# Kernel optimization log

Measured on AMD Instinct MI355X. Metric: run time of the kernel, lower is better.

## Reference

```python
import jax, jax.numpy as jnp
import numpy as np

B, E, DIN, H, D, T = 16, 512, 1024, 8, 128, 3
NEG = -1e30
LRELU_SLOPE = 0.2


def setup_inputs() -> dict:
    key = jax.random.key(0)
    ks = jax.random.split(key, 6)
    x = jax.random.normal(ks[0], (B, E, DIN), dtype=jnp.float32)
    adj = jax.random.randint(ks[1], (B, E, E), 0, 4, dtype=jnp.int32)  # 0=no edge, 1..3 edge types
    node_mask = jnp.ones((B, E, 1), dtype=jnp.float32)
    W = jax.random.normal(ks[2], (H, T, DIN, D), dtype=jnp.float32) * 0.02
    a1 = jax.random.normal(ks[3], (H, T, D), dtype=jnp.float32) * 0.02  # a[:d]
    a2 = jax.random.normal(ks[4], (H, T, D), dtype=jnp.float32) * 0.02  # a[d:]
    return {"x": x, "adj": adj, "node_mask": node_mask, "W": W, "a1": a1, "a2": a2}


def reference(x, adj, node_mask, W, a1, a2):
    # h per head/type: [H, T, B, E, D]
    h = jnp.einsum('bei,htid->htbed', x, W)
    # a(cat(h_i, h_j)) = h_i . a1 + h_j . a2 (linear, no bias)
    left = jnp.einsum('htbed,htd->htbe', h, a1)   # [H,T,B,E]
    right = jnp.einsum('htbed,htd->htbe', h, a2)  # [H,T,B,E]
    score = left[..., :, None] + right[..., None, :]             # [H,T,B,E,E]
    score = jnp.where(score > 0, score, LRELU_SLOPE * score)      # LeakyReLU(0.2)
    type_ids = (jnp.arange(T, dtype=adj.dtype) + 1).reshape(1, T, 1, 1, 1)
    # sum over types: only positions where adj == type contribute
    scores = jnp.sum(jnp.where(adj[None, None] == type_ids, score, 0.0), axis=1)  # [H,B,E,E]
    scores = jnp.where(adj[None] > 0, scores, NEG)
    coefs = jax.nn.softmax(scores, axis=-1)                       # [H,B,E,E]
    # original bug (faithful): h used in aggregation is from the LAST edge type
    h_last = h[:, -1] * node_mask[None]                           # [H,B,E,D]
    out = jnp.einsum('hbef,hbfd->hbed', coefs, h_last)            # [H,B,E,D]
    out = jnp.transpose(out, (1, 2, 0, 3)).reshape(B, E, H * D)   # concat heads
    return jax.nn.relu(out)
```

## Files before the change

### kernel.cpp

```cpp
#include <hip/hip_runtime.h>

typedef __attribute__((ext_vector_type(8))) _Float16 half8;
typedef __attribute__((ext_vector_type(8))) unsigned short u16x8;
typedef __attribute__((ext_vector_type(4))) unsigned short u16x4;
typedef __attribute__((ext_vector_type(4))) float f32x4;

#define NEGV (-1e30f)


__device__ __forceinline__ unsigned short f2h(float f) {
    union { _Float16 h; unsigned short u; } c;
    c.h = (_Float16)f;
    return c.u;
}
__device__ __forceinline__ float h2f(unsigned short u) {
    union { _Float16 h; unsigned short u; } c;
    c.u = u;
    return (float)c.h;
}

__global__ __launch_bounds__(256) void pack_all(const float* __restrict__ W,
                                                const float* __restrict__ a1,
                                                const float* __restrict__ a2,
                                                unsigned short* __restrict__ Bf) {
    __shared__ float tile[64 * 133];
    const int bid = blockIdx.x;
    const int tid = threadIdx.x;

    if (bid < 128) {
        const int kt = bid & 15, h = bid >> 4;
        const int k0 = kt * 64;
        const float* wsrc = W + ((size_t)((h * 3 + 2) * 1024) + k0) * 128;

        #pragma unroll
        for (int rep = 0; rep < 8; ++rep) {
            int idx = rep * 256 + tid;
            int k = idx >> 5, dc = (idx & 31) * 4;
            float4 v = *(const float4*)(wsrc + (size_t)k * 128 + dc);
            tile[k * 133 + dc + 0] = v.x;
            tile[k * 133 + dc + 1] = v.y;
            tile[k * 133 + dc + 2] = v.z;
            tile[k * 133 + dc + 3] = v.w;
        }
        __syncthreads();
        #pragma unroll
        for (int rep = 0; rep < 4; ++rep) {
            int idx = rep * 256 + tid;
            int d = idx >> 3, kc = (idx & 7) * 8;
            u16x8 vh;
            #pragma unroll
            for (int q = 0; q < 8; ++q) vh[q] = f2h(tile[(kc + q) * 133 + d]);
            *(u16x8*)(Bf + (size_t)(h * 128 + d) * 1024 + k0 + kc) = vh;
        }
    } else if (bid < 512) {
        const int b2 = bid - 128;
        const int kt = b2 & 15, ht = b2 >> 4;
        const int h = ht & 7, t = ht >> 3;
        const int k0 = kt * 64;
        const float* wsrc = W + ((size_t)((h * 3 + t) * 1024) + k0) * 128;

        #pragma unroll
        for (int rep = 0; rep < 8; ++rep) {
            int idx = rep * 256 + tid;
            int k = idx >> 5, dc = (idx & 31) * 4;
            float4 v = *(const float4*)(wsrc + (size_t)k * 128 + dc);
            tile[k * 133 + dc + 0] = v.x;
            tile[k * 133 + dc + 1] = v.y;
            tile[k * 133 + dc + 2] = v.z;
            tile[k * 133 + dc + 3] = v.w;
        }
        __syncthreads();
        if (tid < 128) {
            const int k = tid & 63, s = tid >> 6;
            const float* ar = (s ? a2 : a1) + (h * 3 + t) * 128;
            float acc = 0.f;
            #pragma unroll 4
            for (int d = 0; d < 128; ++d) acc += tile[k * 133 + d] * ar[d];
            Bf[(size_t)(1024 + s * 24 + t * 8 + h) * 1024 + k0 + k] = f2h(acc);
        }
    } else {
        const int n = 1072 + (bid - 512);
        *(unsigned long long*)(Bf + (size_t)n * 1024 + tid * 4) = 0ull;
    }
}

__global__ __launch_bounds__(256, 3) void mgemm(const float* __restrict__ X,
                                                const unsigned short* __restrict__ Bf,
                                                const float* __restrict__ nm,
                                                unsigned short* __restrict__ Vt,
                                                float* __restrict__ LR) {
    __shared__ unsigned short Ah[128 * 32];
    __shared__ unsigned short Al[128 * 32];
    __shared__ unsigned short Bfs[128 * 32];

    const int bid = blockIdx.x;
    const int swz = (bid & 7) * 72 + (bid >> 3);
    const int nt = swz % 9, mt = swz / 9;
    const int n0 = nt * 128, m0 = mt * 128;

    const int tid = threadIdx.x;
    const int lane = tid & 63, w = tid >> 6;
    const int wr = w >> 1, wc = w & 1;
    const int fr = lane & 15, fq = lane >> 4;

    f32x4 acc[4][4];
    #pragma unroll
    for (int m = 0; m < 4; ++m)
        #pragma unroll
        for (int n = 0; n < 4; ++n) acc[m][n] = (f32x4){0.f, 0.f, 0.f, 0.f};

    const int arow = tid >> 1, ahalf = tid & 1;
    const float* xs = X + (size_t)(m0 + arow) * 1024 + ahalf * 16;
    unsigned short* adh = Ah + arow * 32 + ahalf * 16;
    unsigned short* adl = Al + arow * 32 + ahalf * 16;

    for (int k0 = 0; k0 < 1024; k0 += 32) {
        __syncthreads();

        #pragma unroll
        for (int q = 0; q < 2; ++q) {
            const int s = q * 256 + tid;
            const int brow = s >> 2, bkb = s & 3;
            const unsigned short* g = Bf + (size_t)(n0 + brow) * 1024 + k0 + bkb * 8;
            unsigned short* d = Bfs + (q * 256 + w * 64) * 8;
            __builtin_amdgcn_global_load_lds(
                (const __attribute__((address_space(1))) void*)g,
                (__attribute__((address_space(3))) void*)d, 16, 0, 0);
        }

        float xf[16];
        #pragma unroll
        for (int i = 0; i < 4; ++i) {
            float4 v = *(const float4*)(xs + k0 + i * 4);
            xf[i * 4 + 0] = v.x; xf[i * 4 + 1] = v.y;
            xf[i * 4 + 2] = v.z; xf[i * 4 + 3] = v.w;
        }
        u16x8 vh0, vh1, vl0, vl1;
        #pragma unroll
        for (int i = 0; i < 8; ++i) {
            unsigned short hi = f2h(xf[i]);
            vh0[i] = hi;
            vl0[i] = f2h(xf[i] - h2f(hi));
        }
        #pragma unroll
        for (int i = 0; i < 8; ++i) {
            unsigned short hi = f2h(xf[8 + i]);
            vh1[i] = hi;
            vl1[i] = f2h(xf[8 + i] - h2f(hi));
        }
        *(u16x8*)(adh) = vh0;
        *(u16x8*)(adh + 8) = vh1;
        *(u16x8*)(adl) = vl0;
        *(u16x8*)(adl + 8) = vl1;

        __syncthreads();

        half8 amh[4], bn[4];
        #pragma unroll
        for (int m = 0; m < 4; ++m)
            amh[m] = *(half8*)(Ah + (wr * 64 + m * 16 + fr) * 32 + fq * 8);
        #pragma unroll
        for (int n = 0; n < 4; ++n)
            bn[n] = *(half8*)(Bfs + (wc * 64 + n * 16 + fr) * 32 + fq * 8);
        #pragma unroll
        for (int m = 0; m < 4; ++m)
            #pragma unroll
            for (int n = 0; n < 4; ++n)
                acc[m][n] = __builtin_amdgcn_mfma_f32_16x16x32_f16(amh[m], bn[n], acc[m][n], 0, 0, 0);

        half8 aml[4];
        #pragma unroll
        for (int m = 0; m < 4; ++m)
            aml[m] = *(half8*)(Al + (wr * 64 + m * 16 + fr) * 32 + fq * 8);
        #pragma unroll
        for (int m = 0; m < 4; ++m)
            #pragma unroll
            for (int n = 0; n < 4; ++n)
                acc[m][n] = __builtin_amdgcn_mfma_f32_16x16x32_f16(aml[m], bn[n], acc[m][n], 0, 0, 0);
    }

    if (nt < 8) {
        const int b_ = (mt * 128) >> 9;
        const int jb0 = (mt & 3) * 128;
        unsigned short* vtw = Vt + (size_t)(nt * 16 + b_) * 128 * 512;
        #pragma unroll
        for (int m = 0; m < 4; ++m) {
            const int jb = jb0 + wr * 64 + m * 16 + fq * 4;
            float mk[4];
            #pragma unroll
            for (int r = 0; r < 4; ++r)
                mk[r] = nm[m0 + wr * 64 + m * 16 + fq * 4 + r];
            #pragma unroll
            for (int n = 0; n < 4; ++n) {
                const int d = wc * 64 + n * 16 + fr;
                u16x4 pk;
                #pragma unroll
                for (int r = 0; r < 4; ++r) pk[r] = f2h(acc[m][n][r] * mk[r]);
                *(u16x4*)(vtw + (size_t)d * 512 + jb) = pk;
            }
        }
    } else {
        #pragma unroll
        for (int m = 0; m < 4; ++m) {
            #pragma unroll
            for (int r = 0; r < 4; ++r) {
                const int R = m0 + wr * 64 + m * 16 + fq * 4 + r;
                #pragma unroll
                for (int n = 0; n < 4; ++n) {
                    const int c = wc * 64 + n * 16 + fr;
                    if (c < 48) LR[(size_t)c * 8192 + R] = acc[m][n][r];
                }
            }
        }
    }
}

__global__ __launch_bounds__(256) void adjb_kernel(const int* __restrict__ adj,
                                                   unsigned char* __restrict__ adjB) {
    const int idx = blockIdx.x * 256 + threadIdx.x;
    const int4* s = (const int4*)(adj + (size_t)idx * 16);
    int4 v0 = s[0], v1 = s[1], v2 = s[2], v3 = s[3];
    union { unsigned char c[16]; int4 v; } o;
    o.c[0] = (unsigned char)v0.x; o.c[1] = (unsigned char)v0.y;
    o.c[2] = (unsigned char)v0.z; o.c[3] = (unsigned char)v0.w;
    o.c[4] = (unsigned char)v1.x; o.c[5] = (unsigned char)v1.y;
    o.c[6] = (unsigned char)v1.z; o.c[7] = (unsigned char)v1.w;
    o.c[8] = (unsigned char)v2.x; o.c[9] = (unsigned char)v2.y;
    o.c[10] = (unsigned char)v2.z; o.c[11] = (unsigned char)v2.w;
    o.c[12] = (unsigned char)v3.x; o.c[13] = (unsigned char)v3.y;
    o.c[14] = (unsigned char)v3.z; o.c[15] = (unsigned char)v3.w;
    *(int4*)(adjB + (size_t)idx * 16) = o.v;
}

__global__ __launch_bounds__(256, 4) void attn_kernel(const unsigned short* __restrict__ Vt,
                                                      const float* __restrict__ LR,
                                                      const unsigned char* __restrict__ adjB,
                                                      float* __restrict__ out) {
    __shared__ __align__(16) unsigned short Vb[2][16 * 512];
    __shared__ __align__(16) float rt[3 * 512];

    const int bid = blockIdx.x;
    const int itg = bid >> 7, hb = bid & 127, h = hb >> 4, b = hb & 15;
    const int tid = threadIdx.x, w = tid >> 6, lane = tid & 63;
    const int fr = lane & 15, fq = lane >> 4;
    const int i0 = (itg * 4 + w) * 16;
    const int fq8 = fq * 8;

    for (int idx = tid; idx < 1536; idx += 256) {
        int t = idx >> 9, j = idx & 511;
        rt[idx] = LR[(size_t)(24 + t * 8 + h) * 8192 + b * 512 + j];
    }
    const float lf0 = LR[(size_t)(h) * 8192 + b * 512 + i0 + fr];
    const float lf1 = LR[(size_t)(8 + h) * 8192 + b * 512 + i0 + fr];
    const float lf2 = LR[(size_t)(16 + h) * 8192 + b * 512 + i0 + fr];
    const unsigned char* arow = adjB + (size_t)(b * 512 + i0 + fr) * 512;
    const unsigned short* vt = Vt + (size_t)(h * 16 + b) * 128 * 512;

#define STAGE_V(bufp, os_) do {                                                   \
        _Pragma("unroll")                                                          \
        for (int q_ = 0; q_ < 4; ++q_) {                                           \
            const int nh_ = q_ * 4 + w;                                            \
            const unsigned short* src_ = vt + (size_t)((nh_ >> 1) * 16 + fr) * 512 \
                                          + (os_) * 64 + (nh_ & 1) * 32 + fq8;     \
            unsigned short* dst_ = (bufp) + nh_ * 512;                             \
            __builtin_amdgcn_global_load_lds(                                      \
                (const __attribute__((address_space(1))) void*)src_,               \
                (__attribute__((address_space(3))) void*)dst_, 16, 0, 0);          \
        }                                                                          \
    } while (0)

    STAGE_V(&Vb[0][0], 0);
    uint2 aA = *(const uint2*)(arow + fq8);
    uint2 aB = *(const uint2*)(arow + fq8 + 32);

    f32x4 acc[8];
    #pragma unroll
    for (int n = 0; n < 8; ++n) acc[n] = (f32x4){0.f, 0.f, 0.f, 0.f};
    float rsum = 0.f;

    __syncthreads();

    #pragma unroll 1
    for (int os = 0; os < 8; ++os) {
        unsigned short* vb = &Vb[os & 1][0];
        if (os < 7) STAGE_V(&Vb[(os & 1) ^ 1][0], os + 1);

        const int jA = os * 64 + fq8;
        const int jB = jA + 32;

        u16x8 vhA, vlA, vhB, vlB;
        {
            float4 r0a = *(const float4*)(rt + jA), r0b = *(const float4*)(rt + jA + 4);
            float4 r1a = *(const float4*)(rt + 512 + jA), r1b = *(const float4*)(rt + 512 + jA + 4);
            float4 r2a = *(const float4*)(rt + 1024 + jA), r2b = *(const float4*)(rt + 1024 + jA + 4);
            float e0[8] = {r0a.x, r0a.y, r0a.z, r0a.w, r0b.x, r0b.y, r0b.z, r0b.w};
            float e1[8] = {r1a.x, r1a.y, r1a.z, r1a.w, r1b.x, r1b.y, r1b.z, r1b.w};
            float e2[8] = {r2a.x, r2a.y, r2a.z, r2a.w, r2b.x, r2b.y, r2b.z, r2b.w};
            #pragma unroll
            for (int q = 0; q < 8; ++q) {
                unsigned av = ((q < 4 ? aA.x : aA.y) >> (8 * (q & 3))) & 255u;
                float sb = (av == 1u) ? (lf0 + e0[q])
                         : (av == 2u) ? (lf1 + e1[q]) : (lf2 + e2[q]);
                float sv = fmaxf(sb, 0.f) + 0.2f * fminf(sb, 0.f);
                float p = (av != 0u) ? __expf(sv) : 0.f;
                rsum += p;
                unsigned short hi = f2h(p);
                vhA[q] = hi;
                vlA[q] = f2h(p - h2f(hi));
            }
        }
        {
            float4 r0a = *(const float4*)(rt + jB), r0b = *(const float4*)(rt + jB + 4);
            float4 r1a = *(const float4*)(rt + 512 + jB), r1b = *(const float4*)(rt + 512 + jB + 4);
            float4 r2a = *(const float4*)(rt + 1024 + jB), r2b = *(const float4*)(rt + 1024 + jB + 4);
            float e0[8] = {r0a.x, r0a.y, r0a.z, r0a.w, r0b.x, r0b.y, r0b.z, r0b.w};
            float e1[8] = {r1a.x, r1a.y, r1a.z, r1a.w, r1b.x, r1b.y, r1b.z, r1b.w};
            float e2[8] = {r2a.x, r2a.y, r2a.z, r2a.w, r2b.x, r2b.y, r2b.z, r2b.w};
            #pragma unroll
            for (int q = 0; q < 8; ++q) {
                unsigned av = ((q < 4 ? aB.x : aB.y) >> (8 * (q & 3))) & 255u;
                float sb = (av == 1u) ? (lf0 + e0[q])
                         : (av == 2u) ? (lf1 + e1[q]) : (lf2 + e2[q]);
                float sv = fmaxf(sb, 0.f) + 0.2f * fminf(sb, 0.f);
                float p = (av != 0u) ? __expf(sv) : 0.f;
                rsum += p;
                unsigned short hi = f2h(p);
                vhB[q] = hi;
                vlB[q] = f2h(p - h2f(hi));
            }
        }
        if (os < 7) {
            aA = *(const uint2*)(arow + (os + 1) * 64 + fq8);
            aB = *(const uint2*)(arow + (os + 1) * 64 + fq8 + 32);
        }

        half8 ahA = *(half8*)&vhA, alA = *(half8*)&vlA;
        half8 ahB = *(half8*)&vhB, alB = *(half8*)&vlB;

        #pragma unroll
        for (int n = 0; n < 8; ++n) {
            half8 vA = *(half8*)(vb + (n * 2 + 0) * 512 + lane * 8);
            half8 vB = *(half8*)(vb + (n * 2 + 1) * 512 + lane * 8);
            acc[n] = __builtin_amdgcn_mfma_f32_16x16x32_f16(ahA, vA, acc[n], 0, 0, 0);
            acc[n] = __builtin_amdgcn_mfma_f32_16x16x32_f16(alA, vA, acc[n], 0, 0, 0);
            acc[n] = __builtin_amdgcn_mfma_f32_16x16x32_f16(ahB, vB, acc[n], 0, 0, 0);
            acc[n] = __builtin_amdgcn_mfma_f32_16x16x32_f16(alB, vB, acc[n], 0, 0, 0);
        }
        __syncthreads();
    }
#undef STAGE_V

    rsum += __shfl_xor(rsum, 16);
    rsum += __shfl_xor(rsum, 32);

    #pragma unroll
    for (int rr = 0; rr < 4; ++rr) {
        const int row = fq * 4 + rr;
        const float inv = 1.0f / __shfl(rsum, row);
        #pragma unroll
        for (int n = 0; n < 8; ++n) {
            out[(size_t)(b * 512 + i0 + row) * 1024 + h * 128 + n * 16 + fr] =
                fmaxf(acc[n][rr] * inv, 0.f);
        }
    }
}

extern "C" void kernel_launch(void* const* d_in, const int* in_sizes, int n_in,
                              void* d_out, int out_size, void* d_ws, size_t ws_size,
                              hipStream_t stream) {
    const float* x   = (const float*)d_in[0];
    const int*   adj = (const int*)d_in[1];
    const float* nm  = (const float*)d_in[2];
    const float* W   = (const float*)d_in[3];
    const float* a1  = (const float*)d_in[4];
    const float* a2  = (const float*)d_in[5];
    float* out = (float*)d_out;
    char* wsb = (char*)d_ws;

    unsigned short* Bf   = (unsigned short*)(wsb);
    float*          LR   = (float*)(wsb + 21495808);
    unsigned short* Vt   = (unsigned short*)(wsb + 23068672);
    unsigned char*  adjB = (unsigned char*)(wsb + 39845888);

    hipLaunchKernelGGL(adjb_kernel, dim3(1024), dim3(256), 0, stream, adj, adjB);
    hipLaunchKernelGGL(pack_all, dim3(592), dim3(256), 0, stream, W, a1, a2, Bf);
    hipLaunchKernelGGL(mgemm, dim3(576), dim3(256), 0, stream, x, Bf, nm, Vt, LR);
    hipLaunchKernelGGL(attn_kernel, dim3(1024), dim3(256), 0, stream, Vt, LR, adjB, out);
}
```

Measured before the change: 119.8 us.

## Double-buffer LDS tiles in mgemm to overlap next-tile loads with MFMA

Splits the A-hi, A-lo and B shared-memory tiles into two buffers. The next K-slice's B tile (async global-to-LDS load) and X values are fetched before the current slice's MFMAs run, and the fp16 split conversion is written afterwards. One barrier per iteration replaces two. LDS per block doubles to 48KB, which may limit the requested 3 blocks per CU and raise register pressure from the extra float4s held across the MFMAs.

```diff
diff --git a/kernel.cpp b/kernel.cpp
--- a/kernel.cpp
+++ b/kernel.cpp
@@ -89,9 +89,9 @@
                                                 const float* __restrict__ nm,
                                                 unsigned short* __restrict__ Vt,
                                                 float* __restrict__ LR) {
-    __shared__ unsigned short Ah[128 * 32];
-    __shared__ unsigned short Al[128 * 32];
-    __shared__ unsigned short Bfs[128 * 32];
+    __shared__ unsigned short Ah[2][128 * 32];
+    __shared__ unsigned short Al[2][128 * 32];
+    __shared__ unsigned short Bfs[2][128 * 32];
 
     const int bid = blockIdx.x;
     const int swz = (bid & 7) * 72 + (bid >> 3);
@@ -111,57 +111,81 @@
 
     const int arow = tid >> 1, ahalf = tid & 1;
     const float* xs = X + (size_t)(m0 + arow) * 1024 + ahalf * 16;
-    unsigned short* adh = Ah + arow * 32 + ahalf * 16;
-    unsigned short* adl = Al + arow * 32 + ahalf * 16;
+    const int aoff = arow * 32 + ahalf * 16;
+
+#define GLDB(kk, buf) do {                                                        \
+        _Pragma("unroll")                                                          \
+        for (int q_ = 0; q_ < 2; ++q_) {                                           \
+            const int s_ = q_ * 256 + tid;                                         \
+            const int brow_ = s_ >> 2, bkb_ = s_ & 3;                              \
+            const unsigned short* g_ = Bf + (size_t)(n0 + brow_) * 1024 + (kk) + bkb_ * 8; \
+            unsigned short* d_ = &Bfs[buf][(q_ * 256 + w * 64) * 8];               \
+            __builtin_amdgcn_global_load_lds(                                      \
+                (const __attribute__((address_space(1))) void*)g_,                 \
+                (__attribute__((address_space(3))) void*)d_, 16, 0, 0);            \
+        }                                                                          \
+    } while (0)
+
+#define CONVA(xa_, xb_, buf) do {                                                 \
+        float xf_[8] = {(xa_).x, (xa_).y, (xa_).z, (xa_).w,                        \
+                        (xb_).x, (xb_).y, (xb_).z, (xb_).w};                       \
+        u16x8 vh_, vl_;                                                            \
+        _Pragma("unroll")                                                          \
+        for (int i_ = 0; i_ < 8; ++i_) {                                           \
+            unsigned short hi_ = f2h(xf_[i_]);                                     \
+            vh_[i_] = hi_;                                                         \
+            vl_[i_] = f2h(xf_[i_] - h2f(hi_));                                     \
+        }                                                                          \
+        *(u16x8*)(&Ah[buf][aoff]) = vh_;                                           \
+        *(u16x8*)(&Al[buf][aoff]) = vl_;                                           \
+    } while (0)
+
+#define CONVA2(xa_, xb_, buf) do {                                                \
+        float xf_[8] = {(xa_).x, (xa_).y, (xa_).z, (xa_).w,                        \
+                        (xb_).x, (xb_).y, (xb_).z, (xb_).w};                       \
+        u16x8 vh_, vl_;                                                            \
+        _Pragma("unroll")                                                          \
+        for (int i_ = 0; i_ < 8; ++i_) {                                           \
+            unsigned short hi_ = f2h(xf_[i_]);                                     \
+            vh_[i_] = hi_;                                                         \
+            vl_[i_] = f2h(xf_[i_] - h2f(hi_));                                     \
+        }                                                                          \
+        *(u16x8*)(&Ah[buf][aoff + 8]) = vh_;                                       \
+        *(u16x8*)(&Al[buf][aoff + 8]) = vl_;                                       \
+    } while (0)
+
+    GLDB(0, 0);
+    {
+        float4 xa = *(const float4*)(xs);
+        float4 xb = *(const float4*)(xs + 4);
+        float4 xc = *(const float4*)(xs + 8);
+        float4 xd = *(const float4*)(xs + 12);
+        CONVA(xa, xb, 0);
+        CONVA2(xc, xd, 0);
+    }
+    __syncthreads();
 
     for (int k0 = 0; k0 < 1024; k0 += 32) {
-        __syncthreads();
-
-        #pragma unroll
-        for (int q = 0; q < 2; ++q) {
-            const int s = q * 256 + tid;
-            const int brow = s >> 2, bkb = s & 3;
-            const unsigned short* g = Bf + (size_t)(n0 + brow) * 1024 + k0 + bkb * 8;
-            unsigned short* d = Bfs + (q * 256 + w * 64) * 8;
-            __builtin_amdgcn_global_load_lds(
-                (const __attribute__((address_space(1))) void*)g,
-                (__attribute__((address_space(3))) void*)d, 16, 0, 0);
-        }
-
-        float xf[16];
-        #pragma unroll
-        for (int i = 0; i < 4; ++i) {
-            float4 v = *(const float4*)(xs + k0 + i * 4);
-            xf[i * 4 + 0] = v.x; xf[i * 4 + 1] = v.y;
-            xf[i * 4 + 2] = v.z; xf[i * 4 + 3] = v.w;
-        }
-        u16x8 vh0, vh1, vl0, vl1;
-        #pragma unroll
-        for (int i = 0; i < 8; ++i) {
-            unsigned short hi = f2h(xf[i]);
-            vh0[i] = hi;
-            vl0[i] = f2h(xf[i] - h2f(hi));
-        }
-        #pragma unroll
-        for (int i = 0; i < 8; ++i) {
-            unsigned short hi = f2h(xf[8 + i]);
-            vh1[i] = hi;
-            vl1[i] = f2h(xf[8 + i] - h2f(hi));
-        }
-        *(u16x8*)(adh) = vh0;
-        *(u16x8*)(adh + 8) = vh1;
-        *(u16x8*)(adl) = vl0;
-        *(u16x8*)(adl + 8) = vl1;
-
-        __syncthreads();
+        const int cur = (k0 >> 5) & 1;
+        const int nxt = cur ^ 1;
+        const bool more = (k0 < 992);
+
+        float4 xa, xb, xc, xd;
+        if (more) {
+            GLDB(k0 + 32, nxt);
+            xa = *(const float4*)(xs + k0 + 32);
+            xb = *(const float4*)(xs + k0 + 36);
+            xc = *(const float4*)(xs + k0 + 40);
+            xd = *(const float4*)(xs + k0 + 44);
+        }
 
         half8 amh[4], bn[4];
         #pragma unroll
         for (int m = 0; m < 4; ++m)
-            amh[m] = *(half8*)(Ah + (wr * 64 + m * 16 + fr) * 32 + fq * 8);
+            amh[m] = *(half8*)(&Ah[cur][(wr * 64 + m * 16 + fr) * 32 + fq * 8]);
         #pragma unroll
         for (int n = 0; n < 4; ++n)
-            bn[n] = *(half8*)(Bfs + (wc * 64 + n * 16 + fr) * 32 + fq * 8);
+            bn[n] = *(half8*)(&Bfs[cur][(wc * 64 + n * 16 + fr) * 32 + fq * 8]);
         #pragma unroll
         for (int m = 0; m < 4; ++m)
             #pragma unroll
@@ -171,13 +195,23 @@
         half8 aml[4];
         #pragma unroll
         for (int m = 0; m < 4; ++m)
-            aml[m] = *(half8*)(Al + (wr * 64 + m * 16 + fr) * 32 + fq * 8);
+            aml[m] = *(half8*)(&Al[cur][(wr * 64 + m * 16 + fr) * 32 + fq * 8]);
         #pragma unroll
         for (int m = 0; m < 4; ++m)
             #pragma unroll
             for (int n = 0; n < 4; ++n)
                 acc[m][n] = __builtin_amdgcn_mfma_f32_16x16x32_f16(aml[m], bn[n], acc[m][n], 0, 0, 0);
-    }
+
+        if (more) {
+            CONVA(xa, xb, nxt);
+            CONVA2(xc, xd, nxt);
+        }
+
+        __syncthreads();
+    }
+#undef GLDB
+#undef CONVA
+#undef CONVA2
 
     if (nt < 8) {
         const int b_ = (mt * 128) >> 9;
```

Result: faster. 116.9 us (-2.4%).
